# Kernel tuning notes

Hardware: AMD Instinct MI355X
Metric: run time of the kernel (lower is better)

Reference implementation:

```python
import jax, jax.numpy as jnp
import numpy as np

B, T, C, HS = 1024, 128, 384, 64


def setup_inputs() -> dict:
    key = jax.random.key(0)
    k1, k2, k3, k4 = jax.random.split(key, 4)
    std = 1.0 / np.sqrt(C)  # ~ nn.Linear default init scale
    return {
        "x": jax.random.normal(k1, (B, T, C), dtype=jnp.float32),
        "Wq": jax.random.normal(k2, (C, HS), dtype=jnp.float32) * std,
        "Wk": jax.random.normal(k3, (C, HS), dtype=jnp.float32) * std,
        "Wv": jax.random.normal(k4, (C, HS), dtype=jnp.float32) * std,
    }


def reference(x, Wq, Wk, Wv):
    # x: [B, T, C]; Wq/Wk/Wv: [C, HS]
    q = jnp.einsum("btc,ch->bth", x, Wq)
    k = jnp.einsum("btc,ch->bth", x, Wk)
    v = jnp.einsum("btc,ch->bth", x, Wv)
    scale = 1.0 / jnp.sqrt(jnp.asarray(k.shape[-1], dtype=x.dtype))
    wei = jnp.einsum("bth,bsh->bts", q, k) * scale  # [B, T, T]
    t = x.shape[1]
    causal = jnp.tril(jnp.ones((t, t), dtype=bool))
    wei = jnp.where(causal, wei, jnp.asarray(-jnp.inf, dtype=wei.dtype))
    wei = jax.nn.softmax(wei, axis=-1)
    # dropout omitted (eval mode / deterministic reference)
    out = jnp.einsum("bts,bsh->bth", wei, v)  # [B, T, HS]
    return out
```

## Files before the change

### kernel.cpp

```cpp
#include <hip/hip_runtime.h>


typedef __attribute__((ext_vector_type(8)))  short  short8;
typedef __attribute__((ext_vector_type(16))) float  floatx16;
typedef __attribute__((ext_vector_type(4)))  float  float4v;

#define T_DIM   128
#define C_DIM   384
#define HS      64
#define NCHUNK  12
#define SLAB    1536

#define QK_PITCH 68
#define V_PITCH  132
#define P_PITCH  132
#define Q_OFF 0
#define K_OFF 17408
#define V_OFF 34816
#define LDS_BYTES 51712
#define P_OFF 0

#define MFMA(a,b,c) __builtin_amdgcn_mfma_f32_32x32x16_bf16((a),(b),(c),0,0,0)

__device__ inline unsigned short f2bf(float f){
    unsigned u = __builtin_bit_cast(unsigned, f);
    u += 0x7FFFu + ((u >> 16) & 1u);
    return (unsigned short)(u >> 16);
}

__device__ inline short8 ld_b64x2(const char* p){
    union { unsigned long long u[2]; short8 s; } r;
    r.u[0] = *(const unsigned long long*)(p);
    r.u[1] = *(const unsigned long long*)(p + 8);
    return r.s;
}

__global__ void prep_wt(const float* __restrict__ Wq, const float* __restrict__ Wk,
                        const float* __restrict__ Wv, unsigned short* __restrict__ wt){
    int idx = blockIdx.x * 256 + threadIdx.x;
    if (idx >= 48 * SLAB) return;
    int slab = idx / SLAB;
    int rem  = idx - slab * SLAB;
    int n = rem >> 3, j = rem & 7;
    int half = slab & 1, ks = (slab >> 1) & 1, c = slab >> 2;
    int kg = c*32 + ks*16 + half*8 + j;
    const float* W = (n < 64) ? Wq : (n < 128) ? Wk : Wv;
    wt[idx] = f2bf(W[kg * HS + (n & 63)]);
}

__launch_bounds__(256, 2)
__global__ void attn_kernel(const float* __restrict__ x,
                            const unsigned short* __restrict__ wtg,
                            float* __restrict__ out){
    __shared__ __align__(16) char smem[LDS_BYTES];
    const int tid  = threadIdx.x;
    const int lane = tid & 63;
    const int wave = tid >> 6;
    const int l31  = lane & 31;
    const int half = lane >> 5;
    const int koff = half * 8;
    const int b    = blockIdx.x;
    const float* xb = x + (size_t)b * (T_DIM * C_DIM);

    const int mpair = wave & 1;
    const int ntri  = wave >> 1;
    const int mrow0 = 64 * mpair + l31;
    const short8* wf = (const short8*)wtg;
    const int nbase = 96 * ntri + l31;

    floatx16 acc[6] = {};
    float4v bufA[8], bufB[8];

    auto xload = [&](float4v (&buf)[8], int c){
        #pragma unroll
        for (int ks = 0; ks < 2; ++ks)
            #pragma unroll
            for (int mbl = 0; mbl < 2; ++mbl){
                const float* g = xb + (mrow0 + 32*mbl)*C_DIM + (c*32 + ks*16 + koff);
                buf[ks*4+mbl*2+0] = *(const float4v*)g;
                buf[ks*4+mbl*2+1] = *(const float4v*)(g + 4);
            }
    };
    auto body = [&](int c, float4v (&cur)[8], float4v (&nxt)[8]){
        if (c + 1 < NCHUNK) xload(nxt, c + 1);
        short8 afrag[2][2];
        #pragma unroll
        for (int ks = 0; ks < 2; ++ks)
            #pragma unroll
            for (int mbl = 0; mbl < 2; ++mbl){
                float4v lo = cur[ks*4+mbl*2+0], hi = cur[ks*4+mbl*2+1];
                short8 a;
                a[0]=(short)f2bf(lo[0]); a[1]=(short)f2bf(lo[1]);
                a[2]=(short)f2bf(lo[2]); a[3]=(short)f2bf(lo[3]);
                a[4]=(short)f2bf(hi[0]); a[5]=(short)f2bf(hi[1]);
                a[6]=(short)f2bf(hi[2]); a[7]=(short)f2bf(hi[3]);
                afrag[ks][mbl] = a;
            }
        #pragma unroll
        for (int ks = 0; ks < 2; ++ks){
            const short8* slab = wf + ((c*2 + ks)*2 + half) * 192;
            #pragma unroll
            for (int nbl = 0; nbl < 3; ++nbl){
                short8 bfrag = slab[nbase + 32*nbl];
                acc[nbl*2+0] = MFMA(afrag[ks][0], bfrag, acc[nbl*2+0]);
                acc[nbl*2+1] = MFMA(afrag[ks][1], bfrag, acc[nbl*2+1]);
            }
        }
    };

    xload(bufA, 0);
    for (int cc = 0; cc < NCHUNK; cc += 2){
        body(cc,     bufA, bufB);
        body(cc + 1, bufB, bufA);
    }

    const float QSCALE = 0.125f * 1.44269504088896f;
    #pragma unroll
    for (int nbl = 0; nbl < 3; ++nbl)
        #pragma unroll
        for (int mbl = 0; mbl < 2; ++mbl){
            floatx16 A = acc[nbl*2+mbl];
            int nb = 3*ntri + nbl;
            int mb = 2*mpair + mbl;
            if (nb < 4){
                int base  = (nb < 2) ? Q_OFF : K_OFF;
                int col   = 32 * (nb & 1) + l31;
                float sc  = (nb < 2) ? QSCALE : 1.0f;
                char* bp  = smem + base + col * 2;
                #pragma unroll
                for (int r = 0; r < 16; ++r){
                    int t = 32*mb + (r&3) + 8*(r>>2) + 4*half;
                    *(unsigned short*)(bp + t * (QK_PITCH*2)) = f2bf(A[r] * sc);
                }
            } else {
                int h = 32*(nb-4) + l31;
                char* bp = smem + V_OFF + h * (V_PITCH*2);
                #pragma unroll
                for (int g = 0; g < 4; ++g){
                    int t0 = 32*mb + 8*g + 4*half;
                    union { unsigned short s[4]; unsigned long long u; } pk;
                    pk.s[0]=f2bf(A[4*g+0]); pk.s[1]=f2bf(A[4*g+1]);
                    pk.s[2]=f2bf(A[4*g+2]); pk.s[3]=f2bf(A[4*g+3]);
                    *(unsigned long long*)(bp + t0*2) = pk.u;
                }
            }
        }
    __syncthreads();

    floatx16 accS[4] = {};
    #pragma unroll
    for (int ks = 0; ks < 4; ++ks){
        short8 aq = ld_b64x2(smem + Q_OFF + (32*wave + l31)*(QK_PITCH*2) + (ks*16 + koff)*2);
        #pragma unroll
        for (int st = 0; st < 4; ++st)
            if (st <= wave){
                short8 bk = ld_b64x2(smem + K_OFF + (32*st + l31)*(QK_PITCH*2) + (ks*16 + koff)*2);
                accS[st] = MFMA(aq, bk, accS[st]);
            }
    }
    #pragma unroll
    for (int st = 0; st < 4; ++st)
        if (st <= wave){
            #pragma unroll
            for (int r = 0; r < 16; ++r){
                int trow = (r&3) + 8*(r>>2) + 4*half;
                float e = exp2f(accS[st][r]);
                if (st == wave && l31 > trow) e = 0.0f;
                accS[st][r] = e;
            }
        }

    float linv[16];
    #pragma unroll
    for (int r = 0; r < 16; ++r){
        float l = accS[0][r] + accS[1][r] + accS[2][r] + accS[3][r];
        #pragma unroll
        for (int m = 1; m <= 16; m <<= 1)
            l += __shfl_xor(l, m);
        linv[r] = 1.0f / l;
    }
    __syncthreads();

    #pragma unroll
    for (int st = 0; st < 4; ++st)
        if (st <= wave){
            char* bp = smem + P_OFF + (32*st + l31) * 2;
            #pragma unroll
            for (int r = 0; r < 16; ++r){
                int t = 32*wave + (r&3) + 8*(r>>2) + 4*half;
                *(unsigned short*)(bp + t * (P_PITCH*2)) = f2bf(accS[st][r]);
            }
        }
    __syncthreads();

    floatx16 accO0 = {}, accO1 = {};
    const int nks = 2 * (wave + 1);
    #pragma unroll
    for (int ks = 0; ks < 8; ++ks)
        if (ks < nks){
            short8 ap  = ld_b64x2(smem + P_OFF + (32*wave + l31)*(P_PITCH*2) + (ks*16 + koff)*2);
            short8 bv0 = ld_b64x2(smem + V_OFF + l31        *(V_PITCH*2) + (ks*16 + koff)*2);
            short8 bv1 = ld_b64x2(smem + V_OFF + (l31 + 32) *(V_PITCH*2) + (ks*16 + koff)*2);
            accO0 = MFMA(ap, bv0, accO0);
            accO1 = MFMA(ap, bv1, accO1);
        }

    float* ob = out + (size_t)b * (T_DIM * HS);
    #pragma unroll
    for (int r = 0; r < 16; ++r){
        int t = 32*wave + (r&3) + 8*(r>>2) + 4*half;
        ob[t*HS + l31]      = accO0[r] * linv[r];
        ob[t*HS + l31 + 32] = accO1[r] * linv[r];
    }
}

extern "C" void kernel_launch(void* const* d_in, const int* in_sizes, int n_in,
                              void* d_out, int out_size, void* d_ws, size_t ws_size,
                              hipStream_t stream){
    const float* x  = (const float*)d_in[0];
    const float* Wq = (const float*)d_in[1];
    const float* Wk = (const float*)d_in[2];
    const float* Wv = (const float*)d_in[3];
    unsigned short* wt = (unsigned short*)d_ws;

    prep_wt<<<288, 256, 0, stream>>>(Wq, Wk, Wv, wt);
    attn_kernel<<<1024, 256, 0, stream>>>(x, wt, (float*)d_out);
}
```

Before: 316.3 us.

## Give each wave a full 32-row QKV projection strip and raise occupancy hint

Changes the projection work split from 2 row-blocks × 3 column-blocks per wave to one 32-row strip × all 6 column-blocks per wave. Each wave now converts x only once per row, with half the x prefetch registers, but loads every weight fragment. This cuts x conversion and register pressure and allows launch_bounds of 3 blocks per CU. In exchange, per-wave weight-fragment global loads double, and the higher occupancy target may cause spills.

```diff
diff --git a/kernel.cpp b/kernel.cpp
--- a/kernel.cpp
+++ b/kernel.cpp
@@ -48,7 +48,7 @@
     wt[idx] = f2bf(W[kg * HS + (n & 63)]);
 }
 
-__launch_bounds__(256, 2)
+__launch_bounds__(256, 3)
 __global__ void attn_kernel(const float* __restrict__ x,
                             const unsigned short* __restrict__ wtg,
                             float* __restrict__ out){
@@ -62,48 +62,40 @@
     const int b    = blockIdx.x;
     const float* xb = x + (size_t)b * (T_DIM * C_DIM);
 
-    const int mpair = wave & 1;
-    const int ntri  = wave >> 1;
-    const int mrow0 = 64 * mpair + l31;
+    const float* xrow = xb + (32*wave + l31) * C_DIM;
     const short8* wf = (const short8*)wtg;
-    const int nbase = 96 * ntri + l31;
 
     floatx16 acc[6] = {};
-    float4v bufA[8], bufB[8];
-
-    auto xload = [&](float4v (&buf)[8], int c){
-        #pragma unroll
-        for (int ks = 0; ks < 2; ++ks)
-            #pragma unroll
-            for (int mbl = 0; mbl < 2; ++mbl){
-                const float* g = xb + (mrow0 + 32*mbl)*C_DIM + (c*32 + ks*16 + koff);
-                buf[ks*4+mbl*2+0] = *(const float4v*)g;
-                buf[ks*4+mbl*2+1] = *(const float4v*)(g + 4);
-            }
+    float4v bufA[4], bufB[4];
+
+    auto xload = [&](float4v (&buf)[4], int c){
+        #pragma unroll
+        for (int ks = 0; ks < 2; ++ks){
+            const float* g = xrow + (c*32 + ks*16 + koff);
+            buf[ks*2+0] = *(const float4v*)g;
+            buf[ks*2+1] = *(const float4v*)(g + 4);
+        }
     };
-    auto body = [&](int c, float4v (&cur)[8], float4v (&nxt)[8]){
+    auto body = [&](int c, float4v (&cur)[4], float4v (&nxt)[4]){
         if (c + 1 < NCHUNK) xload(nxt, c + 1);
-        short8 afrag[2][2];
-        #pragma unroll
-        for (int ks = 0; ks < 2; ++ks)
-            #pragma unroll
-            for (int mbl = 0; mbl < 2; ++mbl){
-                float4v lo = cur[ks*4+mbl*2+0], hi = cur[ks*4+mbl*2+1];
-                short8 a;
-                a[0]=(short)f2bf(lo[0]); a[1]=(short)f2bf(lo[1]);
-                a[2]=(short)f2bf(lo[2]); a[3]=(short)f2bf(lo[3]);
-                a[4]=(short)f2bf(hi[0]); a[5]=(short)f2bf(hi[1]);
-                a[6]=(short)f2bf(hi[2]); a[7]=(short)f2bf(hi[3]);
-                afrag[ks][mbl] = a;
-            }
+        short8 afrag[2];
+        #pragma unroll
+        for (int ks = 0; ks < 2; ++ks){
+            float4v lo = cur[ks*2+0], hi = cur[ks*2+1];
+            short8 a;
+            a[0]=(short)f2bf(lo[0]); a[1]=(short)f2bf(lo[1]);
+            a[2]=(short)f2bf(lo[2]); a[3]=(short)f2bf(lo[3]);
+            a[4]=(short)f2bf(hi[0]); a[5]=(short)f2bf(hi[1]);
+            a[6]=(short)f2bf(hi[2]); a[7]=(short)f2bf(hi[3]);
+            afrag[ks] = a;
+        }
         #pragma unroll
         for (int ks = 0; ks < 2; ++ks){
             const short8* slab = wf + ((c*2 + ks)*2 + half) * 192;
             #pragma unroll
-            for (int nbl = 0; nbl < 3; ++nbl){
-                short8 bfrag = slab[nbase + 32*nbl];
-                acc[nbl*2+0] = MFMA(afrag[ks][0], bfrag, acc[nbl*2+0]);
-                acc[nbl*2+1] = MFMA(afrag[ks][1], bfrag, acc[nbl*2+1]);
+            for (int nbl = 0; nbl < 6; ++nbl){
+                short8 bfrag = slab[32*nbl + l31];
+                acc[nbl] = MFMA(afrag[ks], bfrag, acc[nbl]);
             }
         }
     };
@@ -116,35 +108,31 @@
 
     const float QSCALE = 0.125f * 1.44269504088896f;
     #pragma unroll
-    for (int nbl = 0; nbl < 3; ++nbl)
-        #pragma unroll
-        for (int mbl = 0; mbl < 2; ++mbl){
-            floatx16 A = acc[nbl*2+mbl];
-            int nb = 3*ntri + nbl;
-            int mb = 2*mpair + mbl;
-            if (nb < 4){
-                int base  = (nb < 2) ? Q_OFF : K_OFF;
-                int col   = 32 * (nb & 1) + l31;
-                float sc  = (nb < 2) ? QSCALE : 1.0f;
-                char* bp  = smem + base + col * 2;
-                #pragma unroll
-                for (int r = 0; r < 16; ++r){
-                    int t = 32*mb + (r&3) + 8*(r>>2) + 4*half;
-                    *(unsigned short*)(bp + t * (QK_PITCH*2)) = f2bf(A[r] * sc);
-                }
-            } else {
-                int h = 32*(nb-4) + l31;
-                char* bp = smem + V_OFF + h * (V_PITCH*2);
-                #pragma unroll
-                for (int g = 0; g < 4; ++g){
-                    int t0 = 32*mb + 8*g + 4*half;
-                    union { unsigned short s[4]; unsigned long long u; } pk;
-                    pk.s[0]=f2bf(A[4*g+0]); pk.s[1]=f2bf(A[4*g+1]);
-                    pk.s[2]=f2bf(A[4*g+2]); pk.s[3]=f2bf(A[4*g+3]);
-                    *(unsigned long long*)(bp + t0*2) = pk.u;
-                }
-            }
-        }
+    for (int nb = 0; nb < 6; ++nb){
+        floatx16 A = acc[nb];
+        if (nb < 4){
+            int base  = (nb < 2) ? Q_OFF : K_OFF;
+            int col   = 32 * (nb & 1) + l31;
+            float sc  = (nb < 2) ? QSCALE : 1.0f;
+            char* bp  = smem + base + col * 2;
+            #pragma unroll
+            for (int r = 0; r < 16; ++r){
+                int t = 32*wave + (r&3) + 8*(r>>2) + 4*half;
+                *(unsigned short*)(bp + t * (QK_PITCH*2)) = f2bf(A[r] * sc);
+            }
+        } else {
+            int h = 32*(nb-4) + l31;
+            char* bp = smem + V_OFF + h * (V_PITCH*2);
+            #pragma unroll
+            for (int g = 0; g < 4; ++g){
+                int t0 = 32*wave + 8*g + 4*half;
+                union { unsigned short s[4]; unsigned long long u; } pk;
+                pk.s[0]=f2bf(A[4*g+0]); pk.s[1]=f2bf(A[4*g+1]);
+                pk.s[2]=f2bf(A[4*g+2]); pk.s[3]=f2bf(A[4*g+3]);
+                *(unsigned long long*)(bp + t0*2) = pk.u;
+            }
+        }
+    }
     __syncthreads();
 
     floatx16 accS[4] = {};
```

New measurement: 329.1 us. +4.1%, slower.
